# Kernel tuning notes

Measured on AMD Instinct MI355X. Metric: run time of the kernel, lower is better.

## Reference

```python
import jax, jax.numpy as jnp
import numpy as np

GAMMA = 0.99
LAMDA = 0.95
EPS = 1e-8
T = 16777216  # number of steps


def setup_inputs() -> dict:
    key = jax.random.key(0)
    k1, k2, k3 = jax.random.split(key, 3)
    rewards = jax.random.normal(k1, (T,), dtype=jnp.float32)
    v_pred = jax.random.normal(k2, (T + 1,), dtype=jnp.float32)
    dones = jax.random.randint(k3, (T,), 0, 2, dtype=jnp.int32)
    return {"rewards": rewards, "v_pred": v_pred, "dones": dones}


def reference(rewards, v_pred, dones):
    not_done = 1.0 - dones.astype(rewards.dtype)  # [T]
    # TD residual with reset at done: delta_k = r_k + gamma*V_{k+1}*(1-done_k) - V_k
    delta = rewards + GAMMA * v_pred[1:] * not_done - v_pred[:-1]
    # continuation coefficient: adv_k = delta_k + gamma*lamda*(1-done_k)*adv_{k+1}
    cont = (GAMMA * LAMDA) * not_done

    def step(carry, xs):
        d, c = xs
        a = d + c * carry
        return a, a

    _, adv = jax.lax.scan(step, jnp.zeros((), rewards.dtype), (delta, cont), reverse=True)
    # standardize (stateless): (x - mean) / (std + eps)
    adv = (adv - jnp.mean(adv)) / (jnp.std(adv) + EPS)
    return adv
```

## Files before the change

### kernel.cpp

```cpp
#include <hip/hip_runtime.h>


#define GAMMA_F 0.99f
#define GL_F 0.9405f
#define EPS_F 1e-8f

constexpr int NT = 256;
constexpr int SEG = 16;
constexpr int CHUNK = NT * SEG;

__device__ __forceinline__ void load_seg(const float* __restrict__ r,
                                         const float* __restrict__ v,
                                         const int* __restrict__ dn,
                                         int s, float* delta, float* cont) {
    float4 rr[4], vv[4];
    int4 dd[4];
#pragma unroll
    for (int i = 0; i < 4; ++i) {
        rr[i] = ((const float4*)(r + s))[i];
        vv[i] = ((const float4*)(v + s))[i];
        dd[i] = ((const int4*)(dn + s))[i];
    }
    float va[SEG + 1];
#pragma unroll
    for (int i = 0; i < 4; ++i) {
        va[4 * i + 0] = vv[i].x; va[4 * i + 1] = vv[i].y;
        va[4 * i + 2] = vv[i].z; va[4 * i + 3] = vv[i].w;
    }
    va[SEG] = v[s + SEG];
#pragma unroll
    for (int i = 0; i < 4; ++i) {
        float r0[4] = {rr[i].x, rr[i].y, rr[i].z, rr[i].w};
        int   d0[4] = {dd[i].x, dd[i].y, dd[i].z, dd[i].w};
#pragma unroll
        for (int j = 0; j < 4; ++j) {
            int k = 4 * i + j;
            float nd = 1.0f - (float)d0[j];
            delta[k] = r0[j] + GAMMA_F * va[k + 1] * nd - va[k];
            cont[k]  = GL_F * nd;
        }
    }
}

__device__ __forceinline__ void block_rscan(float D, float C, float* Ds, float* Cs, int t) {
    Ds[t] = D; Cs[t] = C;
    __syncthreads();
    for (int off = 1; off < NT; off <<= 1) {
        float d2 = 0.f, c2 = 0.f;
        bool act = (t + off) < NT;
        if (act) { d2 = Ds[t + off]; c2 = Cs[t + off]; }
        __syncthreads();
        if (act) { float a = Ds[t] + Cs[t] * d2; float b = Cs[t] * c2; Ds[t] = a; Cs[t] = b; }
        __syncthreads();
    }
}

__global__ __launch_bounds__(NT) void k_chunk_affine(const float* __restrict__ r,
                                                     const float* __restrict__ v,
                                                     const int* __restrict__ dn,
                                                     float2* __restrict__ aff) {
    const int t = threadIdx.x;
    const int s = blockIdx.x * CHUNK + t * SEG;
    float delta[SEG], cont[SEG];
    load_seg(r, v, dn, s, delta, cont);
    float D = 0.f, C = 1.f;
#pragma unroll
    for (int i = SEG - 1; i >= 0; --i) { D = delta[i] + cont[i] * D; C *= cont[i]; }
    __shared__ float Ds[NT], Cs[NT];
    block_rscan(D, C, Ds, Cs, t);
    if (t == 0) aff[blockIdx.x] = make_float2(Ds[0], Cs[0]);
}

__global__ __launch_bounds__(NT) void k_chunk_scan(const float2* __restrict__ aff,
                                                   float* __restrict__ carry, int nchunk) {
    const int t = threadIdx.x;
    const int per = nchunk / NT;
    const int s = t * per;
    float D = 0.f, C = 1.f;
    for (int i = per - 1; i >= 0; --i) { float2 a = aff[s + i]; D = a.x + a.y * D; C *= a.y; }
    __shared__ float Ds[NT], Cs[NT];
    block_rscan(D, C, Ds, Cs, t);
    float x = (t + 1 < NT) ? Ds[t + 1] : 0.f;
    for (int i = per - 1; i >= 0; --i) {
        int c = s + i;
        float2 a = aff[c];
        carry[c] = x;
        x = a.x + a.y * x;
    }
}

__global__ __launch_bounds__(NT) void k_final(const float* __restrict__ r,
                                              const float* __restrict__ v,
                                              const int* __restrict__ dn,
                                              const float* __restrict__ carry,
                                              float* __restrict__ out,
                                              double2* __restrict__ partial) {
    const int t = threadIdx.x;
    const int chunk = blockIdx.x;
    const int s = chunk * CHUNK + t * SEG;
    float delta[SEG], cont[SEG];
    load_seg(r, v, dn, s, delta, cont);
    float D = 0.f, C = 1.f;
#pragma unroll
    for (int i = SEG - 1; i >= 0; --i) { D = delta[i] + cont[i] * D; C *= cont[i]; }
    __shared__ float Ds[NT], Cs[NT];
    block_rscan(D, C, Ds, Cs, t);
    float cc = carry[chunk];
    float x = (t + 1 < NT) ? (Ds[t + 1] + Cs[t + 1] * cc) : cc;
    float adv[SEG];
    float lsum = 0.f, lsq = 0.f;
#pragma unroll
    for (int i = SEG - 1; i >= 0; --i) {
        x = delta[i] + cont[i] * x;
        adv[i] = x;
        lsum += x;
        lsq += x * x;
    }
#pragma unroll
    for (int i = 0; i < 4; ++i)
        ((float4*)(out + s))[i] = make_float4(adv[4*i], adv[4*i+1], adv[4*i+2], adv[4*i+3]);

    double dsum = (double)lsum, dsq = (double)lsq;
    for (int off = 32; off > 0; off >>= 1) {
        dsum += __shfl_down(dsum, off, 64);
        dsq  += __shfl_down(dsq,  off, 64);
    }
    __shared__ double Ssum[NT / 64], Ssq[NT / 64];
    const int wave = t >> 6, lane = t & 63;
    if (lane == 0) { Ssum[wave] = dsum; Ssq[wave] = dsq; }
    __syncthreads();
    if (t == 0) {
        double a = 0.0, b = 0.0;
        for (int w = 0; w < NT / 64; ++w) { a += Ssum[w]; b += Ssq[w]; }
        partial[chunk] = make_double2(a, b);
    }
}

__global__ __launch_bounds__(NT) void k_stats(const double2* __restrict__ partial,
                                              int nchunk, float2* __restrict__ meanstd,
                                              long long T) {
    const int t = threadIdx.x;
    double a = 0.0, b = 0.0;
    for (int i = t; i < nchunk; i += NT) { double2 p = partial[i]; a += p.x; b += p.y; }
    for (int off = 32; off > 0; off >>= 1) {
        a += __shfl_down(a, off, 64);
        b += __shfl_down(b, off, 64);
    }
    __shared__ double Sa[NT / 64], Sb[NT / 64];
    const int wave = t >> 6, lane = t & 63;
    if (lane == 0) { Sa[wave] = a; Sb[wave] = b; }
    __syncthreads();
    if (t == 0) {
        double s = 0.0, q = 0.0;
        for (int w = 0; w < NT / 64; ++w) { s += Sa[w]; q += Sb[w]; }
        double mean = s / (double)T;
        double var = q / (double)T - mean * mean;
        double sd = sqrt(var > 0.0 ? var : 0.0);
        meanstd[0] = make_float2((float)mean, (float)(1.0 / (sd + (double)EPS_F)));
    }
}

__global__ __launch_bounds__(NT) void k_norm(float* __restrict__ out,
                                             const float2* __restrict__ meanstd,
                                             int n4) {
    const float2 ms = *meanstd;
    float4* o4 = (float4*)out;
    int i = blockIdx.x * blockDim.x + threadIdx.x;
    const int stride = gridDim.x * blockDim.x;
    for (; i < n4; i += stride) {
        float4 v = o4[i];
        v.x = (v.x - ms.x) * ms.y;
        v.y = (v.y - ms.x) * ms.y;
        v.z = (v.z - ms.x) * ms.y;
        v.w = (v.w - ms.x) * ms.y;
        o4[i] = v;
    }
}

extern "C" void kernel_launch(void* const* d_in, const int* in_sizes, int n_in,
                              void* d_out, int out_size, void* d_ws, size_t ws_size,
                              hipStream_t stream) {
    const float* rewards = (const float*)d_in[0];
    const float* v_pred  = (const float*)d_in[1];
    const int*   dones   = (const int*)d_in[2];
    float* out = (float*)d_out;
    const long long T = in_sizes[0];
    const int nchunk = (int)(T / CHUNK);

    char* ws = (char*)d_ws;
    float2*  aff     = (float2*)ws;
    float*   carry   = (float*)(ws + (size_t)nchunk * 8);
    double2* partial = (double2*)(ws + (size_t)nchunk * 12);
    float2*  meanstd = (float2*)(ws + (size_t)nchunk * 12 + (size_t)nchunk * 16);

    hipLaunchKernelGGL(k_chunk_affine, dim3(nchunk), dim3(NT), 0, stream,
                       rewards, v_pred, dones, aff);
    hipLaunchKernelGGL(k_chunk_scan, dim3(1), dim3(NT), 0, stream, aff, carry, nchunk);
    hipLaunchKernelGGL(k_final, dim3(nchunk), dim3(NT), 0, stream,
                       rewards, v_pred, dones, carry, out, partial);
    hipLaunchKernelGGL(k_stats, dim3(1), dim3(NT), 0, stream, partial, nchunk, meanstd, T);
    hipLaunchKernelGGL(k_norm, dim3(2048), dim3(NT), 0, stream, out, meanstd, (int)(T / 4));
}
```

Before: 114.9 us.

## Switch scan kernels to coalesced per-lane float4 layout with wave-shuffle scans

Each lane now handles four contiguous elements, so a wave reads contiguous memory with one float4 load per lane instead of four strided float4 loads per thread over 16 elements. The shared-memory block scan with many barriers is replaced by an in-wave shuffle scan plus a small four-wave combine. Chunks shrink from 4096 to 1024 elements, which quadruples the block count and makes the single-block chunk-scan kernel do four times more serial work per thread. The normalize kernel grid is also doubled.

New measurement: 144.7 us. 25.9% more time.

```diff
diff --git a/kernel.cpp b/kernel.cpp
--- a/kernel.cpp
+++ b/kernel.cpp
@@ -6,39 +6,60 @@
 #define EPS_F 1e-8f
 
 constexpr int NT = 256;
-constexpr int SEG = 16;
-constexpr int CHUNK = NT * SEG;
-
-__device__ __forceinline__ void load_seg(const float* __restrict__ r,
-                                         const float* __restrict__ v,
-                                         const int* __restrict__ dn,
-                                         int s, float* delta, float* cont) {
-    float4 rr[4], vv[4];
-    int4 dd[4];
-#pragma unroll
-    for (int i = 0; i < 4; ++i) {
-        rr[i] = ((const float4*)(r + s))[i];
-        vv[i] = ((const float4*)(v + s))[i];
-        dd[i] = ((const int4*)(dn + s))[i];
-    }
-    float va[SEG + 1];
-#pragma unroll
-    for (int i = 0; i < 4; ++i) {
-        va[4 * i + 0] = vv[i].x; va[4 * i + 1] = vv[i].y;
-        va[4 * i + 2] = vv[i].z; va[4 * i + 3] = vv[i].w;
-    }
-    va[SEG] = v[s + SEG];
-#pragma unroll
-    for (int i = 0; i < 4; ++i) {
-        float r0[4] = {rr[i].x, rr[i].y, rr[i].z, rr[i].w};
-        int   d0[4] = {dd[i].x, dd[i].y, dd[i].z, dd[i].w};
-#pragma unroll
-        for (int j = 0; j < 4; ++j) {
-            int k = 4 * i + j;
-            float nd = 1.0f - (float)d0[j];
-            delta[k] = r0[j] + GAMMA_F * va[k + 1] * nd - va[k];
-            cont[k]  = GL_F * nd;
-        }
+constexpr int PL = 4;
+constexpr int WSPAN = 64 * PL;
+constexpr int CHUNK = 4 * WSPAN;
+
+__device__ __forceinline__ void lane_load(const float* __restrict__ r,
+                                          const float* __restrict__ v,
+                                          const int* __restrict__ dn,
+                                          int e0, int lane,
+                                          float* d, float* c) {
+    float4 rr = *(const float4*)(r + e0);
+    float4 vv = *(const float4*)(v + e0);
+    int4   dd = *(const int4*)(dn + e0);
+    float vnext = __shfl_down(vv.x, 1);
+    if (lane == 63) vnext = v[e0 + PL];
+    float va[5] = {vv.x, vv.y, vv.z, vv.w, vnext};
+    float rf[4] = {rr.x, rr.y, rr.z, rr.w};
+    int   di[4] = {dd.x, dd.y, dd.z, dd.w};
+#pragma unroll
+    for (int i = 0; i < PL; ++i) {
+        float nd = 1.0f - (float)di[i];
+        d[i] = rf[i] + GAMMA_F * va[i + 1] * nd - va[i];
+        c[i] = GL_F * nd;
+    }
+}
+
+__device__ __forceinline__ void lane_group_and_scan(const float* d, const float* c,
+                                                    int lane, float& D, float& C) {
+    D = 0.f; C = 1.f;
+#pragma unroll
+    for (int i = PL - 1; i >= 0; --i) { D = d[i] + c[i] * D; C *= c[i]; }
+#pragma unroll
+    for (int off = 1; off < 64; off <<= 1) {
+        float tD = __shfl_down(D, off);
+        float tC = __shfl_down(C, off);
+        if (lane + off < 64) { D = D + C * tD; C = C * tC; }
+    }
+}
+
+__global__ __launch_bounds__(NT) void k_chunk_affine(const float* __restrict__ r,
+                                                     const float* __restrict__ v,
+                                                     const int* __restrict__ dn,
+                                                     float2* __restrict__ aff) {
+    const int t = threadIdx.x, lane = t & 63, wv = t >> 6;
+    const int e0 = blockIdx.x * CHUNK + wv * WSPAN + lane * PL;
+    float d[PL], c[PL], D, C;
+    lane_load(r, v, dn, e0, lane, d, c);
+    lane_group_and_scan(d, c, lane, D, C);
+    __shared__ float2 waff[4];
+    if (lane == 0) waff[wv] = make_float2(D, C);
+    __syncthreads();
+    if (t == 0) {
+        float BD = 0.f, BC = 1.f;
+        for (int w = 3; w >= 0; --w) { BD = waff[w].x + waff[w].y * BD; BC *= waff[w].y; }
+        aff[blockIdx.x] = make_float2(BD, BC);
     }
 }
 
@@ -53,22 +74,6 @@
         if (act) { float a = Ds[t] + Cs[t] * d2; float b = Cs[t] * c2; Ds[t] = a; Cs[t] = b; }
         __syncthreads();
     }
-}
-
-__global__ __launch_bounds__(NT) void k_chunk_affine(const float* __restrict__ r,
-                                                     const float* __restrict__ v,
-                                                     const int* __restrict__ dn,
-                                                     float2* __restrict__ aff) {
-    const int t = threadIdx.x;
-    const int s = blockIdx.x * CHUNK + t * SEG;
-    float delta[SEG], cont[SEG];
-    load_seg(r, v, dn, s, delta, cont);
-    float D = 0.f, C = 1.f;
-#pragma unroll
-    for (int i = SEG - 1; i >= 0; --i) { D = delta[i] + cont[i] * D; C *= cont[i]; }
-    __shared__ float Ds[NT], Cs[NT];
-    block_rscan(D, C, Ds, Cs, t);
-    if (t == 0) aff[blockIdx.x] = make_float2(Ds[0], Cs[0]);
 }
 
 __global__ __launch_bounds__(NT) void k_chunk_scan(const float2* __restrict__ aff,
@@ -82,9 +87,9 @@
     block_rscan(D, C, Ds, Cs, t);
     float x = (t + 1 < NT) ? Ds[t + 1] : 0.f;
     for (int i = per - 1; i >= 0; --i) {
-        int c = s + i;
-        float2 a = aff[c];
-        carry[c] = x;
+        int cidx = s + i;
+        float2 a = aff[cidx];
+        carry[cidx] = x;
         x = a.x + a.y * x;
     }
 }
@@ -95,44 +100,43 @@
                                               const float* __restrict__ carry,
                                               float* __restrict__ out,
                                               double2* __restrict__ partial) {
-    const int t = threadIdx.x;
-    const int chunk = blockIdx.x;
-    const int s = chunk * CHUNK + t * SEG;
-    float delta[SEG], cont[SEG];
-    load_seg(r, v, dn, s, delta, cont);
-    float D = 0.f, C = 1.f;
-#pragma unroll
-    for (int i = SEG - 1; i >= 0; --i) { D = delta[i] + cont[i] * D; C *= cont[i]; }
-    __shared__ float Ds[NT], Cs[NT];
-    block_rscan(D, C, Ds, Cs, t);
-    float cc = carry[chunk];
-    float x = (t + 1 < NT) ? (Ds[t + 1] + Cs[t + 1] * cc) : cc;
-    float adv[SEG];
-    float lsum = 0.f, lsq = 0.f;
-#pragma unroll
-    for (int i = SEG - 1; i >= 0; --i) {
-        x = delta[i] + cont[i] * x;
-        adv[i] = x;
-        lsum += x;
-        lsq += x * x;
-    }
-#pragma unroll
-    for (int i = 0; i < 4; ++i)
-        ((float4*)(out + s))[i] = make_float4(adv[4*i], adv[4*i+1], adv[4*i+2], adv[4*i+3]);
-
-    double dsum = (double)lsum, dsq = (double)lsq;
+    const int t = threadIdx.x, lane = t & 63, wv = t >> 6;
+    const int blk = blockIdx.x;
+    const int e0 = blk * CHUNK + wv * WSPAN + lane * PL;
+    float d[PL], c[PL], D, C;
+    lane_load(r, v, dn, e0, lane, d, c);
+    lane_group_and_scan(d, c, lane, D, C);
+    __shared__ float2 waff[4];
+    if (lane == 0) waff[wv] = make_float2(D, C);
+    __syncthreads();
+    float cc = carry[blk];
+    float xw = cc;
+    for (int w = 3; w > wv; --w) xw = waff[w].x + waff[w].y * xw;
+    float SD = __shfl_down(D, 1), SC = __shfl_down(C, 1);
+    if (lane == 63) { SD = 0.f; SC = 1.f; }
+    float x = SD + SC * xw;
+    float a[PL];
+    float ls = 0.f, lq = 0.f;
+#pragma unroll
+    for (int i = PL - 1; i >= 0; --i) {
+        x = d[i] + c[i] * x;
+        a[i] = x;
+        ls += x; lq += x * x;
+    }
+    *(float4*)(out + e0) = make_float4(a[0], a[1], a[2], a[3]);
+
+    double s = (double)ls, q = (double)lq;
     for (int off = 32; off > 0; off >>= 1) {
-        dsum += __shfl_down(dsum, off, 64);
-        dsq  += __shfl_down(dsq,  off, 64);
-    }
-    __shared__ double Ssum[NT / 64], Ssq[NT / 64];
-    const int wave = t >> 6, lane = t & 63;
-    if (lane == 0) { Ssum[wave] = dsum; Ssq[wave] = dsq; }
+        s += __shfl_down(s, off);
+        q += __shfl_down(q, off);
+    }
+    __shared__ double Ss[4], Sq[4];
+    if (lane == 0) { Ss[wv] = s; Sq[wv] = q; }
     __syncthreads();
     if (t == 0) {
-        double a = 0.0, b = 0.0;
-        for (int w = 0; w < NT / 64; ++w) { a += Ssum[w]; b += Ssq[w]; }
-        partial[chunk] = make_double2(a, b);
+        double A = 0.0, B = 0.0;
+        for (int w = 0; w < 4; ++w) { A += Ss[w]; B += Sq[w]; }
+        partial[blk] = make_double2(A, B);
     }
 }
 
@@ -143,8 +147,8 @@
     double a = 0.0, b = 0.0;
     for (int i = t; i < nchunk; i += NT) { double2 p = partial[i]; a += p.x; b += p.y; }
     for (int off = 32; off > 0; off >>= 1) {
-        a += __shfl_down(a, off, 64);
-        b += __shfl_down(b, off, 64);
+        a += __shfl_down(a, off);
+        b += __shfl_down(b, off);
     }
     __shared__ double Sa[NT / 64], Sb[NT / 64];
     const int wave = t >> 6, lane = t & 63;
@@ -191,7 +195,7 @@
     float2*  aff     = (float2*)ws;
     float*   carry   = (float*)(ws + (size_t)nchunk * 8);
     double2* partial = (double2*)(ws + (size_t)nchunk * 12);
-    float2*  meanstd = (float2*)(ws + (size_t)nchunk * 12 + (size_t)nchunk * 16);
+    float2*  meanstd = (float2*)(ws + (size_t)nchunk * 28);
 
     hipLaunchKernelGGL(k_chunk_affine, dim3(nchunk), dim3(NT), 0, stream,
                        rewards, v_pred, dones, aff);
@@ -199,5 +203,5 @@
     hipLaunchKernelGGL(k_final, dim3(nchunk), dim3(NT), 0, stream,
                        rewards, v_pred, dones, carry, out, partial);
     hipLaunchKernelGGL(k_stats, dim3(1), dim3(NT), 0, stream, partial, nchunk, meanstd, T);
-    hipLaunchKernelGGL(k_norm, dim3(2048), dim3(NT), 0, stream, out, meanstd, (int)(T / 4));
-}
+    hipLaunchKernelGGL(k_norm, dim3(4096), dim3(NT), 0, stream, out, meanstd, (int)(T / 4));
+}
```

## Compute stats via per-chunk affine moments, fuse normalize, compress dones to bitmasks

Applied to the files above, without the earlier changes.

Replaces the five-kernel pipeline with three kernels. The first pass computes per-chunk affine descriptors and polynomial moments (sum and sum of squares as functions of the incoming carry), and packs the done flags into ballot bitmasks. The single-block scan then derives the exact mean and std without a separate pass over the output. The final pass re-scans each chunk with wave shuffles, applies the normalization inline and writes the output once. This removes the out read-modify-write pass and the 4-byte-per-element dones reread, at the cost of more arithmetic and possible float rounding differences in the moment algebra.

Result: no change. 115.8 us (+0.7%).

```diff
diff --git a/kernel.cpp b/kernel.cpp
--- a/kernel.cpp
+++ b/kernel.cpp
@@ -6,175 +6,217 @@
 #define EPS_F 1e-8f
 
 constexpr int NT = 256;
-constexpr int SEG = 16;
-constexpr int CHUNK = NT * SEG;
-
-__device__ __forceinline__ void load_seg(const float* __restrict__ r,
-                                         const float* __restrict__ v,
-                                         const int* __restrict__ dn,
-                                         int s, float* delta, float* cont) {
-    float4 rr[4], vv[4];
-    int4 dd[4];
-#pragma unroll
-    for (int i = 0; i < 4; ++i) {
-        rr[i] = ((const float4*)(r + s))[i];
-        vv[i] = ((const float4*)(v + s))[i];
-        dd[i] = ((const int4*)(dn + s))[i];
-    }
-    float va[SEG + 1];
-#pragma unroll
-    for (int i = 0; i < 4; ++i) {
-        va[4 * i + 0] = vv[i].x; va[4 * i + 1] = vv[i].y;
-        va[4 * i + 2] = vv[i].z; va[4 * i + 3] = vv[i].w;
-    }
-    va[SEG] = v[s + SEG];
-#pragma unroll
-    for (int i = 0; i < 4; ++i) {
-        float r0[4] = {rr[i].x, rr[i].y, rr[i].z, rr[i].w};
-        int   d0[4] = {dd[i].x, dd[i].y, dd[i].z, dd[i].w};
-#pragma unroll
-        for (int j = 0; j < 4; ++j) {
-            int k = 4 * i + j;
-            float nd = 1.0f - (float)d0[j];
-            delta[k] = r0[j] + GAMMA_F * va[k + 1] * nd - va[k];
-            cont[k]  = GL_F * nd;
-        }
-    }
-}
-
-__device__ __forceinline__ void block_rscan(float D, float C, float* Ds, float* Cs, int t) {
+constexpr int PL = 8;
+constexpr int TILE = 512;
+constexpr int CHUNK = 2 * TILE;
+constexpr int K2T = 1024;
+
+__device__ __forceinline__ void tile_scan(const float4& r0, const float4& r1,
+                                          const float4& v0, const float4& v1,
+                                          const float* nd, float vn63, int lane,
+                                          float* d, float* c,
+                                          float& sD, float& sC, float& S1D, float& S1C) {
+    float vnext = __shfl_down(v0.x, 1);
+    if (lane == 63) vnext = vn63;
+    float va[9] = {v0.x, v0.y, v0.z, v0.w, v1.x, v1.y, v1.z, v1.w, vnext};
+    float rf[8] = {r0.x, r0.y, r0.z, r0.w, r1.x, r1.y, r1.z, r1.w};
+#pragma unroll
+    for (int i = 0; i < 8; ++i) {
+        d[i] = rf[i] + GAMMA_F * va[i + 1] * nd[i] - va[i];
+        c[i] = GL_F * nd[i];
+    }
+    float D = 0.f, C = 1.f;
+#pragma unroll
+    for (int i = 7; i >= 0; --i) { D = d[i] + c[i] * D; C *= c[i]; }
+#pragma unroll
+    for (int off = 1; off < 64; off <<= 1) {
+        float tD = __shfl_down(D, off);
+        float tC = __shfl_down(C, off);
+        if (lane + off < 64) { D = D + C * tD; C = C * tC; }
+    }
+    sD = D; sC = C;
+    S1D = __shfl_down(D, 1); S1C = __shfl_down(C, 1);
+    if (lane == 63) { S1D = 0.f; S1C = 1.f; }
+}
+
+__device__ __forceinline__ void lane_moms(const float* d, const float* c,
+                                          float S1D, float S1C, float* mm) {
+    float x = S1D, P = S1C;
+    float A = 0.f, Pp = 0.f, L2 = 0.f, LP = 0.f, P2 = 0.f;
+#pragma unroll
+    for (int i = 7; i >= 0; --i) {
+        x = d[i] + c[i] * x;
+        P *= c[i];
+        A += x; Pp += P; L2 += x * x; LP += x * P; P2 += P * P;
+    }
+    mm[0] = A; mm[1] = Pp; mm[2] = L2; mm[3] = LP; mm[4] = P2;
+}
+
+__global__ __launch_bounds__(NT) void k_desc(const float* __restrict__ r,
+                                             const float* __restrict__ v,
+                                             const int* __restrict__ dn,
+                                             float2* __restrict__ desc,
+                                             float4* __restrict__ mom4,
+                                             float* __restrict__ mom1,
+                                             unsigned long long* __restrict__ dmask) {
+    const int tid = threadIdx.x, lane = tid & 63, wv = tid >> 6;
+    const int ch = blockIdx.x * 4 + wv;
+    const int base = ch * CHUNK;
+    const int o0 = base + lane * PL, o1 = base + TILE + lane * PL;
+
+    float4 r00 = *(const float4*)(r + o0), r01 = *(const float4*)(r + o0 + 4);
+    float4 v00 = *(const float4*)(v + o0), v01 = *(const float4*)(v + o0 + 4);
+    int4   a00 = *(const int4*)(dn + o0),  a01 = *(const int4*)(dn + o0 + 4);
+    float4 r10 = *(const float4*)(r + o1), r11 = *(const float4*)(r + o1 + 4);
+    float4 v10 = *(const float4*)(v + o1), v11 = *(const float4*)(v + o1 + 4);
+    int4   a10 = *(const int4*)(dn + o1),  a11 = *(const int4*)(dn + o1 + 4);
+
+    float vn63_t1 = (lane == 63) ? v[base + CHUNK] : 0.f;
+    float vn63_t0 = __shfl(v10.x, 0);
+
+    int di0[8] = {a00.x, a00.y, a00.z, a00.w, a01.x, a01.y, a01.z, a01.w};
+    int di1[8] = {a10.x, a10.y, a10.z, a10.w, a11.x, a11.y, a11.z, a11.w};
+    float nd0[8], nd1[8];
+    unsigned long long m0[8], m1[8];
+#pragma unroll
+    for (int i = 0; i < 8; ++i) {
+        nd0[i] = 1.f - (float)di0[i]; m0[i] = __ballot(di0[i] != 0);
+        nd1[i] = 1.f - (float)di1[i]; m1[i] = __ballot(di1[i] != 0);
+    }
+
+    float d1[8], c1[8], sD1, sC1, S1D1, S1C1;
+    tile_scan(r10, r11, v10, v11, nd1, vn63_t1, lane, d1, c1, sD1, sC1, S1D1, S1C1);
+    const float T1D = __shfl(sD1, 0), T1C = __shfl(sC1, 0);
+    float d0[8], c0[8], sD0, sC0, S1D0, S1C0;
+    tile_scan(r00, r01, v00, v01, nd0, vn63_t0, lane, d0, c0, sD0, sC0, S1D0, S1C0);
+    const float T0D = __shfl(sD0, 0), T0C = __shfl(sC0, 0);
+
+    float mm1[5], mm0[5];
+    lane_moms(d1, c1, S1D1, S1C1, mm1);
+    lane_moms(d0, c0, S1D0, S1C0, mm0);
+    const float e = T1D, f = T1C;
+    float gA  = mm1[0] + mm0[0] + e * mm0[1];
+    float gP  = mm1[1] + f * mm0[1];
+    float gL2 = mm1[2] + mm0[2] + 2.f * e * mm0[3] + e * e * mm0[4];
+    float gLP = mm1[3] + f * (mm0[3] + e * mm0[4]);
+    float gP2 = mm1[4] + f * f * mm0[4];
+#pragma unroll
+    for (int off = 32; off > 0; off >>= 1) {
+        gA  += __shfl_down(gA,  off);
+        gP  += __shfl_down(gP,  off);
+        gL2 += __shfl_down(gL2, off);
+        gLP += __shfl_down(gLP, off);
+        gP2 += __shfl_down(gP2, off);
+    }
+    if (lane == 0) {
+        desc[ch] = make_float2(T0D + T0C * T1D, T0C * T1C);
+        mom4[ch] = make_float4(gA, gP, gL2, gLP);
+        mom1[ch] = gP2;
+        unsigned long long* mp = dmask + (size_t)ch * 16;
+#pragma unroll
+        for (int i = 0; i < 8; ++i) { mp[i] = m0[i]; mp[8 + i] = m1[i]; }
+    }
+}
+
+__global__ __launch_bounds__(K2T) void k_scan(const float2* __restrict__ desc,
+                                              const float4* __restrict__ mom4,
+                                              const float* __restrict__ mom1,
+                                              float* __restrict__ carry,
+                                              float2* __restrict__ meanstd,
+                                              int nchunk, long long T) {
+    const int t = threadIdx.x;
+    const int per = nchunk / K2T;
+    const int s = t * per;
+    float D = 0.f, C = 1.f;
+    for (int i = per - 1; i >= 0; --i) { float2 a = desc[s + i]; D = a.x + a.y * D; C *= a.y; }
+    __shared__ float Ds[K2T], Cs[K2T];
     Ds[t] = D; Cs[t] = C;
     __syncthreads();
-    for (int off = 1; off < NT; off <<= 1) {
+    for (int off = 1; off < K2T; off <<= 1) {
         float d2 = 0.f, c2 = 0.f;
-        bool act = (t + off) < NT;
+        bool act = (t + off) < K2T;
         if (act) { d2 = Ds[t + off]; c2 = Cs[t + off]; }
         __syncthreads();
         if (act) { float a = Ds[t] + Cs[t] * d2; float b = Cs[t] * c2; Ds[t] = a; Cs[t] = b; }
         __syncthreads();
     }
-}
-
-__global__ __launch_bounds__(NT) void k_chunk_affine(const float* __restrict__ r,
-                                                     const float* __restrict__ v,
-                                                     const int* __restrict__ dn,
-                                                     float2* __restrict__ aff) {
-    const int t = threadIdx.x;
-    const int s = blockIdx.x * CHUNK + t * SEG;
-    float delta[SEG], cont[SEG];
-    load_seg(r, v, dn, s, delta, cont);
-    float D = 0.f, C = 1.f;
-#pragma unroll
-    for (int i = SEG - 1; i >= 0; --i) { D = delta[i] + cont[i] * D; C *= cont[i]; }
-    __shared__ float Ds[NT], Cs[NT];
-    block_rscan(D, C, Ds, Cs, t);
-    if (t == 0) aff[blockIdx.x] = make_float2(Ds[0], Cs[0]);
-}
-
-__global__ __launch_bounds__(NT) void k_chunk_scan(const float2* __restrict__ aff,
-                                                   float* __restrict__ carry, int nchunk) {
-    const int t = threadIdx.x;
-    const int per = nchunk / NT;
-    const int s = t * per;
-    float D = 0.f, C = 1.f;
-    for (int i = per - 1; i >= 0; --i) { float2 a = aff[s + i]; D = a.x + a.y * D; C *= a.y; }
-    __shared__ float Ds[NT], Cs[NT];
-    block_rscan(D, C, Ds, Cs, t);
-    float x = (t + 1 < NT) ? Ds[t + 1] : 0.f;
+    float x = (t + 1 < K2T) ? Ds[t + 1] : 0.f;
+    double gS = 0.0, gQ = 0.0;
     for (int i = per - 1; i >= 0; --i) {
-        int c = s + i;
-        float2 a = aff[c];
-        carry[c] = x;
+        const int cix = s + i;
+        carry[cix] = x;
+        float4 m = mom4[cix];
+        float p2 = mom1[cix];
+        gS += (double)(m.x + x * m.y);
+        gQ += (double)(m.z + 2.f * x * m.w + x * x * p2);
+        float2 a = desc[cix];
         x = a.x + a.y * x;
     }
-}
-
-__global__ __launch_bounds__(NT) void k_final(const float* __restrict__ r,
-                                              const float* __restrict__ v,
-                                              const int* __restrict__ dn,
-                                              const float* __restrict__ carry,
-                                              float* __restrict__ out,
-                                              double2* __restrict__ partial) {
-    const int t = threadIdx.x;
-    const int chunk = blockIdx.x;
-    const int s = chunk * CHUNK + t * SEG;
-    float delta[SEG], cont[SEG];
-    load_seg(r, v, dn, s, delta, cont);
-    float D = 0.f, C = 1.f;
-#pragma unroll
-    for (int i = SEG - 1; i >= 0; --i) { D = delta[i] + cont[i] * D; C *= cont[i]; }
-    __shared__ float Ds[NT], Cs[NT];
-    block_rscan(D, C, Ds, Cs, t);
-    float cc = carry[chunk];
-    float x = (t + 1 < NT) ? (Ds[t + 1] + Cs[t + 1] * cc) : cc;
-    float adv[SEG];
-    float lsum = 0.f, lsq = 0.f;
-#pragma unroll
-    for (int i = SEG - 1; i >= 0; --i) {
-        x = delta[i] + cont[i] * x;
-        adv[i] = x;
-        lsum += x;
-        lsq += x * x;
-    }
-#pragma unroll
-    for (int i = 0; i < 4; ++i)
-        ((float4*)(out + s))[i] = make_float4(adv[4*i], adv[4*i+1], adv[4*i+2], adv[4*i+3]);
-
-    double dsum = (double)lsum, dsq = (double)lsq;
     for (int off = 32; off > 0; off >>= 1) {
-        dsum += __shfl_down(dsum, off, 64);
-        dsq  += __shfl_down(dsq,  off, 64);
-    }
-    __shared__ double Ssum[NT / 64], Ssq[NT / 64];
-    const int wave = t >> 6, lane = t & 63;
-    if (lane == 0) { Ssum[wave] = dsum; Ssq[wave] = dsq; }
+        gS += __shfl_down(gS, off);
+        gQ += __shfl_down(gQ, off);
+    }
+    __shared__ double Sa[K2T / 64], Sb[K2T / 64];
+    const int wv = t >> 6, lane = t & 63;
+    if (lane == 0) { Sa[wv] = gS; Sb[wv] = gQ; }
     __syncthreads();
     if (t == 0) {
-        double a = 0.0, b = 0.0;
-        for (int w = 0; w < NT / 64; ++w) { a += Ssum[w]; b += Ssq[w]; }
-        partial[chunk] = make_double2(a, b);
-    }
-}
-
-__global__ __launch_bounds__(NT) void k_stats(const double2* __restrict__ partial,
-                                              int nchunk, float2* __restrict__ meanstd,
-                                              long long T) {
-    const int t = threadIdx.x;
-    double a = 0.0, b = 0.0;
-    for (int i = t; i < nchunk; i += NT) { double2 p = partial[i]; a += p.x; b += p.y; }
-    for (int off = 32; off > 0; off >>= 1) {
-        a += __shfl_down(a, off, 64);
-        b += __shfl_down(b, off, 64);
-    }
-    __shared__ double Sa[NT / 64], Sb[NT / 64];
-    const int wave = t >> 6, lane = t & 63;
-    if (lane == 0) { Sa[wave] = a; Sb[wave] = b; }
-    __syncthreads();
-    if (t == 0) {
-        double s = 0.0, q = 0.0;
-        for (int w = 0; w < NT / 64; ++w) { s += Sa[w]; q += Sb[w]; }
-        double mean = s / (double)T;
-        double var = q / (double)T - mean * mean;
+        double S = 0.0, Q = 0.0;
+        for (int w = 0; w < K2T / 64; ++w) { S += Sa[w]; Q += Sb[w]; }
+        double mean = S / (double)T;
+        double var = Q / (double)T - mean * mean;
         double sd = sqrt(var > 0.0 ? var : 0.0);
         meanstd[0] = make_float2((float)mean, (float)(1.0 / (sd + (double)EPS_F)));
     }
 }
 
-__global__ __launch_bounds__(NT) void k_norm(float* __restrict__ out,
-                                             const float2* __restrict__ meanstd,
-                                             int n4) {
-    const float2 ms = *meanstd;
-    float4* o4 = (float4*)out;
-    int i = blockIdx.x * blockDim.x + threadIdx.x;
-    const int stride = gridDim.x * blockDim.x;
-    for (; i < n4; i += stride) {
-        float4 v = o4[i];
-        v.x = (v.x - ms.x) * ms.y;
-        v.y = (v.y - ms.x) * ms.y;
-        v.z = (v.z - ms.x) * ms.y;
-        v.w = (v.w - ms.x) * ms.y;
-        o4[i] = v;
-    }
+__global__ __launch_bounds__(NT) void k_apply(const float* __restrict__ r,
+                                              const float* __restrict__ v,
+                                              const unsigned long long* __restrict__ dmask,
+                                              const float* __restrict__ carry,
+                                              const float2* __restrict__ meanstd,
+                                              float* __restrict__ out) {
+    const int tid = threadIdx.x, lane = tid & 63, wv = tid >> 6;
+    const int ch = blockIdx.x * 4 + wv;
+    const int base = ch * CHUNK;
+    const int o0 = base + lane * PL, o1 = base + TILE + lane * PL;
+
+    float4 r00 = *(const float4*)(r + o0), r01 = *(const float4*)(r + o0 + 4);
+    float4 v00 = *(const float4*)(v + o0), v01 = *(const float4*)(v + o0 + 4);
+    float4 r10 = *(const float4*)(r + o1), r11 = *(const float4*)(r + o1 + 4);
+    float4 v10 = *(const float4*)(v + o1), v11 = *(const float4*)(v + o1 + 4);
+    const unsigned long long* mp = dmask + (size_t)ch * 16;
+
+    float vn63_t1 = (lane == 63) ? v[base + CHUNK] : 0.f;
+    float vn63_t0 = __shfl(v10.x, 0);
+    const float2 ms = meanstd[0];
+    const float cy = carry[ch];
+
+    float nd0[8], nd1[8];
+#pragma unroll
+    for (int i = 0; i < 8; ++i) {
+        nd0[i] = 1.f - (float)((mp[i] >> lane) & 1ull);
+        nd1[i] = 1.f - (float)((mp[8 + i] >> lane) & 1ull);
+    }
+
+    float d1[8], c1[8], sD1, sC1, S1D1, S1C1;
+    tile_scan(r10, r11, v10, v11, nd1, vn63_t1, lane, d1, c1, sD1, sC1, S1D1, S1C1);
+    const float T1D = __shfl(sD1, 0), T1C = __shfl(sC1, 0);
+    float d0[8], c0[8], sD0, sC0, S1D0, S1C0;
+    tile_scan(r00, r01, v00, v01, nd0, vn63_t0, lane, d0, c0, sD0, sC0, S1D0, S1C0);
+
+    float o[8];
+    float x = S1D1 + S1C1 * cy;
+#pragma unroll
+    for (int i = 7; i >= 0; --i) { x = d1[i] + c1[i] * x; o[i] = (x - ms.x) * ms.y; }
+    *(float4*)(out + o1)     = make_float4(o[0], o[1], o[2], o[3]);
+    *(float4*)(out + o1 + 4) = make_float4(o[4], o[5], o[6], o[7]);
+    const float x0e = T1D + T1C * cy;
+    x = S1D0 + S1C0 * x0e;
+#pragma unroll
+    for (int i = 7; i >= 0; --i) { x = d0[i] + c0[i] * x; o[i] = (x - ms.x) * ms.y; }
+    *(float4*)(out + o0)     = make_float4(o[0], o[1], o[2], o[3]);
+    *(float4*)(out + o0 + 4) = make_float4(o[4], o[5], o[6], o[7]);
 }
 
 extern "C" void kernel_launch(void* const* d_in, const int* in_sizes, int n_in,
@@ -188,16 +230,18 @@
     const int nchunk = (int)(T / CHUNK);
 
     char* ws = (char*)d_ws;
-    float2*  aff     = (float2*)ws;
-    float*   carry   = (float*)(ws + (size_t)nchunk * 8);
-    double2* partial = (double2*)(ws + (size_t)nchunk * 12);
-    float2*  meanstd = (float2*)(ws + (size_t)nchunk * 12 + (size_t)nchunk * 16);
-
-    hipLaunchKernelGGL(k_chunk_affine, dim3(nchunk), dim3(NT), 0, stream,
-                       rewards, v_pred, dones, aff);
-    hipLaunchKernelGGL(k_chunk_scan, dim3(1), dim3(NT), 0, stream, aff, carry, nchunk);
-    hipLaunchKernelGGL(k_final, dim3(nchunk), dim3(NT), 0, stream,
-                       rewards, v_pred, dones, carry, out, partial);
-    hipLaunchKernelGGL(k_stats, dim3(1), dim3(NT), 0, stream, partial, nchunk, meanstd, T);
-    hipLaunchKernelGGL(k_norm, dim3(2048), dim3(NT), 0, stream, out, meanstd, (int)(T / 4));
-}
+    float4* mom4 = (float4*)ws;
+    size_t off = (size_t)nchunk * 16;
+    float2* desc = (float2*)(ws + off);  off += (size_t)nchunk * 8;
+    float*  mom1 = (float*)(ws + off);   off += (size_t)nchunk * 4;
+    float*  carry = (float*)(ws + off);  off += (size_t)nchunk * 4;
+    float2* meanstd = (float2*)(ws + off); off += 16;
+    unsigned long long* dmask = (unsigned long long*)(ws + off);
+
+    hipLaunchKernelGGL(k_desc, dim3(nchunk / 4), dim3(NT), 0, stream,
+                       rewards, v_pred, dones, desc, mom4, mom1, dmask);
+    hipLaunchKernelGGL(k_scan, dim3(1), dim3(K2T), 0, stream,
+                       desc, mom4, mom1, carry, meanstd, nchunk, T);
+    hipLaunchKernelGGL(k_apply, dim3(nchunk / 4), dim3(NT), 0, stream,
+                       rewards, v_pred, dmask, carry, meanstd, out);
+}
```
